# Kernel optimization log

Measured on AMD Instinct MI355X. Metric: run time of the kernel, lower is better.

Reference implementation:

```python
import jax, jax.numpy as jnp
import numpy as np

TEMPERATURE = 100.0

def setup_inputs() -> dict:
    key = jax.random.key(0)
    n, d = 8192, 4096
    grad = jax.random.normal(key, (n, d), dtype=jnp.float32)
    return {"grad": grad}

def reference(grad) -> jnp.ndarray:
    # scores_i = sum_j (G @ G^T)_{ij} = G_i . (sum_j G_j)  -- avoids [n,n] gram
    colsum = jnp.sum(grad, axis=0)                 # [d]
    scores = grad @ colsum                         # [n]
    w = jax.nn.softmax(scores / TEMPERATURE, axis=0)  # softmax over rows (dim=0)
    # weighted row pooling: sum_i w_i * G_i -> [d]
    return w @ grad
```

## Files before the change

### kernel.cpp

```cpp
#include <hip/hip_runtime.h>
#include <math.h>

#define NROWS 8192
#define NCOLS 4096
#define NCOLS4 (NCOLS / 4)
#define TEMP_INV 0.01f

#define STRIPS 4
#define CHUNKS 512
#define CHUNK_ROWS (NROWS / CHUNKS)
#define STREAM_BLKS (STRIPS * CHUNKS)

__global__ __launch_bounds__(256)
void colsum_partial_kernel(const float* __restrict__ g,
                           float* __restrict__ partial) {
    const int strip = blockIdx.x & (STRIPS - 1);
    const int chunk = blockIdx.x >> 2;
    const int col   = strip * 1024 + threadIdx.x * 4;
    const float* p  = g + (size_t)chunk * CHUNK_ROWS * NCOLS + col;
    float4 acc = make_float4(0.f, 0.f, 0.f, 0.f);
    #pragma unroll
    for (int r = 0; r < CHUNK_ROWS; ++r) {
        float4 v = *reinterpret_cast<const float4*>(p);
        acc.x += v.x; acc.y += v.y; acc.z += v.z; acc.w += v.w;
        p += NCOLS;
    }
    *reinterpret_cast<float4*>(partial + (size_t)chunk * NCOLS + col) = acc;
}

__global__ __launch_bounds__(256)
void reduce_kernel(const float* __restrict__ partial, float* __restrict__ dst) {
    const int tid = threadIdx.x;
    const int f4  = blockIdx.x * 16 + (tid & 15);
    const int grp = tid >> 4;
    const float4* p4 = reinterpret_cast<const float4*>(partial);
    float4 acc = make_float4(0.f, 0.f, 0.f, 0.f);
    for (int c = grp; c < CHUNKS; c += 16) {
        float4 v = p4[(size_t)c * NCOLS4 + f4];
        acc.x += v.x; acc.y += v.y; acc.z += v.z; acc.w += v.w;
    }
    __shared__ float4 red[256];
    red[tid] = acc;
    __syncthreads();
    #pragma unroll
    for (int s = 128; s >= 16; s >>= 1) {
        if (tid < s) {
            float4 o = red[tid + s];
            red[tid].x += o.x; red[tid].y += o.y;
            red[tid].z += o.z; red[tid].w += o.w;
        }
        __syncthreads();
    }
    if (tid < 16)
        reinterpret_cast<float4*>(dst)[blockIdx.x * 16 + tid] = red[tid];
}

__global__ __launch_bounds__(256)
void scores_kernel(const float* __restrict__ g, const float* __restrict__ colsum,
                   float* __restrict__ scores) {
    __shared__ float4 cs4[NCOLS4];
    for (int i = threadIdx.x; i < NCOLS4; i += 256)
        cs4[i] = reinterpret_cast<const float4*>(colsum)[i];
    __syncthreads();

    const int wave = threadIdx.x >> 6;
    const int lane = threadIdx.x & 63;
    #pragma unroll
    for (int rr = 0; rr < 2; ++rr) {
        const int row = blockIdx.x * 8 + wave * 2 + rr;
        const float4* gp = reinterpret_cast<const float4*>(g)
                         + (size_t)row * NCOLS4;
        float acc = 0.f;
        #pragma unroll
        for (int k = 0; k < 16; ++k) {
            const int idx = k * 64 + lane;
            float4 v = gp[idx];
            float4 c = cs4[idx];
            acc += v.x * c.x + v.y * c.y + v.z * c.z + v.w * c.w;
        }
        #pragma unroll
        for (int off = 32; off; off >>= 1) acc += __shfl_xor(acc, off, 64);
        if (lane == 0) scores[row] = acc;
    }
}

__global__ __launch_bounds__(1024)
void softmax_kernel(const float* __restrict__ scores, float* __restrict__ w) {
    __shared__ float red[16];
    const int tid = threadIdx.x;

    float local[8];
    float m = -INFINITY;
    #pragma unroll
    for (int k = 0; k < 8; ++k) {
        local[k] = scores[tid + k * 1024];
        m = fmaxf(m, local[k]);
    }
    #pragma unroll
    for (int off = 32; off; off >>= 1) m = fmaxf(m, __shfl_xor(m, off, 64));
    if ((tid & 63) == 0) red[tid >> 6] = m;
    __syncthreads();
    float gm = red[0];
    #pragma unroll
    for (int i = 1; i < 16; ++i) gm = fmaxf(gm, red[i]);
    __syncthreads();

    float e[8];
    float s = 0.f;
    #pragma unroll
    for (int k = 0; k < 8; ++k) {
        e[k] = __expf((local[k] - gm) * TEMP_INV);
        s += e[k];
    }
    #pragma unroll
    for (int off = 32; off; off >>= 1) s += __shfl_xor(s, off, 64);
    if ((tid & 63) == 0) red[tid >> 6] = s;
    __syncthreads();
    float total = 0.f;
    #pragma unroll
    for (int i = 0; i < 16; ++i) total += red[i];

    const float inv = 1.0f / total;
    #pragma unroll
    for (int k = 0; k < 8; ++k) w[tid + k * 1024] = e[k] * inv;
}

__global__ __launch_bounds__(256)
void pool_partial_kernel(const float* __restrict__ g, const float* __restrict__ w,
                         float* __restrict__ partial) {
    const int strip = blockIdx.x & (STRIPS - 1);
    const int chunk = blockIdx.x >> 2;

    __shared__ float wsm[CHUNK_ROWS];
    if (threadIdx.x < CHUNK_ROWS)
        wsm[threadIdx.x] = w[chunk * CHUNK_ROWS + threadIdx.x];
    __syncthreads();

    const int col  = strip * 1024 + threadIdx.x * 4;
    const float* p = g + (size_t)chunk * CHUNK_ROWS * NCOLS + col;
    float4 acc = make_float4(0.f, 0.f, 0.f, 0.f);
    #pragma unroll
    for (int r = 0; r < CHUNK_ROWS; ++r) {
        const float wt = wsm[r];
        float4 v = *reinterpret_cast<const float4*>(p);
        acc.x += wt * v.x; acc.y += wt * v.y;
        acc.z += wt * v.z; acc.w += wt * v.w;
        p += NCOLS;
    }
    *reinterpret_cast<float4*>(partial + (size_t)chunk * NCOLS + col) = acc;
}

extern "C" void kernel_launch(void* const* d_in, const int* in_sizes, int n_in,
                              void* d_out, int out_size, void* d_ws, size_t ws_size,
                              hipStream_t stream) {
    const float* grad = (const float*)d_in[0];
    float* out = (float*)d_out;

    float* partial = (float*)d_ws;
    float* colsum  = partial + (size_t)CHUNKS * NCOLS;
    float* scores  = colsum + NCOLS;
    float* wgt     = scores + NROWS;

    colsum_partial_kernel<<<STREAM_BLKS, 256, 0, stream>>>(grad, partial);
    reduce_kernel<<<64, 256, 0, stream>>>(partial, colsum);
    scores_kernel<<<NROWS / 8, 256, 0, stream>>>(grad, colsum, scores);
    softmax_kernel<<<1, 1024, 0, stream>>>(scores, wgt);
    pool_partial_kernel<<<STREAM_BLKS, 256, 0, stream>>>(grad, wgt, partial);
    reduce_kernel<<<64, 256, 0, stream>>>(partial, out);
}
```

Measured before the change: 249.3 us.

## Fuse softmax into pooling kernel and replace final reduction with atomics

Removes the single-block softmax kernel: each pool block recomputes the global max and softmax denominator from all 8192 scores, then builds its own row weights. The pooled partial sums are accumulated straight into the output with float atomics (the output is zeroed inside the scores kernel), so the final reduce kernel is dropped. The chunk count is halved and the scores kernel now handles one row per wave. This cuts two launches and a serialized single-block step. In exchange every block re-reads the 32KB score vector, and atomic contention on the output grows.

```diff
diff --git a/kernel.cpp b/kernel.cpp
--- a/kernel.cpp
+++ b/kernel.cpp
@@ -7,7 +7,7 @@
 #define TEMP_INV 0.01f
 
 #define STRIPS 4
-#define CHUNKS 512
+#define CHUNKS 256
 #define CHUNK_ROWS (NROWS / CHUNKS)
 #define STREAM_BLKS (STRIPS * CHUNKS)
 
@@ -35,6 +35,7 @@
     const int grp = tid >> 4;
     const float4* p4 = reinterpret_cast<const float4*>(partial);
     float4 acc = make_float4(0.f, 0.f, 0.f, 0.f);
+    #pragma unroll 4
     for (int c = grp; c < CHUNKS; c += 16) {
         float4 v = p4[(size_t)c * NCOLS4 + f4];
         acc.x += v.x; acc.y += v.y; acc.z += v.z; acc.w += v.w;
@@ -57,86 +58,84 @@
 
 __global__ __launch_bounds__(256)
 void scores_kernel(const float* __restrict__ g, const float* __restrict__ colsum,
-                   float* __restrict__ scores) {
+                   float* __restrict__ scores, float* __restrict__ out) {
     __shared__ float4 cs4[NCOLS4];
-    for (int i = threadIdx.x; i < NCOLS4; i += 256)
-        cs4[i] = reinterpret_cast<const float4*>(colsum)[i];
+    #pragma unroll
+    for (int k = 0; k < NCOLS4 / 256; ++k)
+        cs4[k * 256 + threadIdx.x] =
+            reinterpret_cast<const float4*>(colsum)[k * 256 + threadIdx.x];
+    if (blockIdx.x < 4)
+        reinterpret_cast<float4*>(out)[blockIdx.x * 256 + threadIdx.x] =
+            make_float4(0.f, 0.f, 0.f, 0.f);
     __syncthreads();
 
     const int wave = threadIdx.x >> 6;
     const int lane = threadIdx.x & 63;
+    const int row  = blockIdx.x * 4 + wave;
+    const float4* gp = reinterpret_cast<const float4*>(g) + (size_t)row * NCOLS4;
+
+    float4 acc = make_float4(0.f, 0.f, 0.f, 0.f);
     #pragma unroll
-    for (int rr = 0; rr < 2; ++rr) {
-        const int row = blockIdx.x * 8 + wave * 2 + rr;
-        const float4* gp = reinterpret_cast<const float4*>(g)
-                         + (size_t)row * NCOLS4;
-        float acc = 0.f;
-        #pragma unroll
-        for (int k = 0; k < 16; ++k) {
-            const int idx = k * 64 + lane;
-            float4 v = gp[idx];
-            float4 c = cs4[idx];
-            acc += v.x * c.x + v.y * c.y + v.z * c.z + v.w * c.w;
-        }
-        #pragma unroll
-        for (int off = 32; off; off >>= 1) acc += __shfl_xor(acc, off, 64);
-        if (lane == 0) scores[row] = acc;
+    for (int k = 0; k < 16; ++k) {
+        const int idx = k * 64 + lane;
+        float4 v = gp[idx];
+        float4 c = cs4[idx];
+        acc.x += v.x * c.x; acc.y += v.y * c.y;
+        acc.z += v.z * c.z; acc.w += v.w * c.w;
     }
-}
-
-__global__ __launch_bounds__(1024)
-void softmax_kernel(const float* __restrict__ scores, float* __restrict__ w) {
-    __shared__ float red[16];
-    const int tid = threadIdx.x;
-
-    float local[8];
-    float m = -INFINITY;
-    #pragma unroll
-    for (int k = 0; k < 8; ++k) {
-        local[k] = scores[tid + k * 1024];
-        m = fmaxf(m, local[k]);
-    }
-    #pragma unroll
-    for (int off = 32; off; off >>= 1) m = fmaxf(m, __shfl_xor(m, off, 64));
-    if ((tid & 63) == 0) red[tid >> 6] = m;
-    __syncthreads();
-    float gm = red[0];
-    #pragma unroll
-    for (int i = 1; i < 16; ++i) gm = fmaxf(gm, red[i]);
-    __syncthreads();
-
-    float e[8];
-    float s = 0.f;
-    #pragma unroll
-    for (int k = 0; k < 8; ++k) {
-        e[k] = __expf((local[k] - gm) * TEMP_INV);
-        s += e[k];
-    }
+    float s = (acc.x + acc.y) + (acc.z + acc.w);
     #pragma unroll
     for (int off = 32; off; off >>= 1) s += __shfl_xor(s, off, 64);
-    if ((tid & 63) == 0) red[tid >> 6] = s;
-    __syncthreads();
-    float total = 0.f;
-    #pragma unroll
-    for (int i = 0; i < 16; ++i) total += red[i];
-
-    const float inv = 1.0f / total;
-    #pragma unroll
-    for (int k = 0; k < 8; ++k) w[tid + k * 1024] = e[k] * inv;
+    if (lane == 0) scores[row] = s;
 }
 
 __global__ __launch_bounds__(256)
-void pool_partial_kernel(const float* __restrict__ g, const float* __restrict__ w,
-                         float* __restrict__ partial) {
+void pool_kernel(const float* __restrict__ g, const float* __restrict__ scores,
+                 float* __restrict__ out) {
+    const int tid   = threadIdx.x;
     const int strip = blockIdx.x & (STRIPS - 1);
     const int chunk = blockIdx.x >> 2;
+    const int wave  = tid >> 6;
+    const int lane  = tid & 63;
 
+    __shared__ float red[8];
     __shared__ float wsm[CHUNK_ROWS];
-    if (threadIdx.x < CHUNK_ROWS)
-        wsm[threadIdx.x] = w[chunk * CHUNK_ROWS + threadIdx.x];
+
+    const float4* s4 = reinterpret_cast<const float4*>(scores);
+    float4 sv[8];
+    float lm = -INFINITY;
+    #pragma unroll
+    for (int k = 0; k < 8; ++k) {
+        sv[k] = s4[k * 256 + tid];
+        lm = fmaxf(lm, fmaxf(fmaxf(sv[k].x, sv[k].y), fmaxf(sv[k].z, sv[k].w)));
+    }
+    #pragma unroll
+    for (int off = 32; off; off >>= 1) lm = fmaxf(lm, __shfl_xor(lm, off, 64));
+    if (lane == 0) red[wave] = lm;
+    __syncthreads();
+    const float m = fmaxf(fmaxf(red[0], red[1]), fmaxf(red[2], red[3]));
+
+    float ls = 0.f;
+    #pragma unroll
+    for (int k = 0; k < 8; ++k) {
+        ls += __expf((sv[k].x - m) * TEMP_INV)
+            + __expf((sv[k].y - m) * TEMP_INV)
+            + __expf((sv[k].z - m) * TEMP_INV)
+            + __expf((sv[k].w - m) * TEMP_INV);
+    }
+    #pragma unroll
+    for (int off = 32; off; off >>= 1) ls += __shfl_xor(ls, off, 64);
+    if (lane == 0) red[4 + wave] = ls;
+    __syncthreads();
+    const float invZ = 1.0f / (red[4] + red[5] + red[6] + red[7]);
+
+    if (tid < CHUNK_ROWS) {
+        const float s = scores[chunk * CHUNK_ROWS + tid];
+        wsm[tid] = __expf((s - m) * TEMP_INV) * invZ;
+    }
     __syncthreads();
 
-    const int col  = strip * 1024 + threadIdx.x * 4;
+    const int col  = strip * 1024 + tid * 4;
     const float* p = g + (size_t)chunk * CHUNK_ROWS * NCOLS + col;
     float4 acc = make_float4(0.f, 0.f, 0.f, 0.f);
     #pragma unroll
@@ -147,7 +146,10 @@
         acc.z += wt * v.z; acc.w += wt * v.w;
         p += NCOLS;
     }
-    *reinterpret_cast<float4*>(partial + (size_t)chunk * NCOLS + col) = acc;
+    atomicAdd(&out[col + 0], acc.x);
+    atomicAdd(&out[col + 1], acc.y);
+    atomicAdd(&out[col + 2], acc.z);
+    atomicAdd(&out[col + 3], acc.w);
 }
 
 extern "C" void kernel_launch(void* const* d_in, const int* in_sizes, int n_in,
@@ -159,12 +161,9 @@
     float* partial = (float*)d_ws;
     float* colsum  = partial + (size_t)CHUNKS * NCOLS;
     float* scores  = colsum + NCOLS;
-    float* wgt     = scores + NROWS;
 
     colsum_partial_kernel<<<STREAM_BLKS, 256, 0, stream>>>(grad, partial);
     reduce_kernel<<<64, 256, 0, stream>>>(partial, colsum);
-    scores_kernel<<<NROWS / 8, 256, 0, stream>>>(grad, colsum, scores);
-    softmax_kernel<<<1, 1024, 0, stream>>>(scores, wgt);
-    pool_partial_kernel<<<STREAM_BLKS, 256, 0, stream>>>(grad, wgt, partial);
-    reduce_kernel<<<64, 256, 0, stream>>>(partial, out);
+    scores_kernel<<<NROWS / 4, 256, 0, stream>>>(grad, colsum, scores, out);
+    pool_kernel<<<STREAM_BLKS, 256, 0, stream>>>(grad, scores, out);
 }
```

Result: no change. 252.0 us (+1.1%).
